# Kernel optimization log

Hardware: AMD Instinct MI355X
Metric: run time of the kernel (lower is better)

Reference implementation:

```python
import jax, jax.numpy as jnp
import numpy as np

ENC, DEC, ATT = 2048, 512, 512

def setup_inputs() -> dict:
    key = jax.random.key(0)
    ks = jax.random.split(key, 8)
    B, L = 64, 1024
    s1 = 1.0 / np.sqrt(ENC)
    s2 = 1.0 / np.sqrt(DEC)
    s3 = 1.0 / np.sqrt(ATT)
    return {
        "features": jax.random.normal(ks[0], (B, L, ENC), jnp.float32),
        "hidden_state": jax.random.normal(ks[1], (B, DEC), jnp.float32),
        "W1": jax.random.uniform(ks[2], (ENC, ATT), jnp.float32, -s1, s1),
        "b1": jax.random.uniform(ks[3], (ATT,), jnp.float32, -s1, s1),
        "W2": jax.random.uniform(ks[4], (DEC, ATT), jnp.float32, -s2, s2),
        "b2": jax.random.uniform(ks[5], (ATT,), jnp.float32, -s2, s2),
        "V": jax.random.uniform(ks[6], (ATT, 1), jnp.float32, -s3, s3),
        "bv": jax.random.uniform(ks[7], (1,), jnp.float32, -s3, s3),
    }

def reference(features, hidden_state, W1, b1, W2, b2, V, bv):
    # features: [B, L, ENC], hidden_state: [B, DEC]
    proj_f = jnp.einsum('ble,ea->bla', features, W1) + b1          # [B, L, A]
    proj_h = (hidden_state @ W2 + b2)[:, None, :]                  # [B, 1, A]
    attention_hidden = jnp.tanh(proj_f + proj_h)                   # [B, L, A]
    score = jnp.einsum('bla,ao->blo', attention_hidden, V) + bv    # [B, L, 1]
    attention_weights = jax.nn.softmax(score, axis=1)              # [B, L, 1]
    context_vector = jnp.sum(attention_weights * features, axis=1) # [B, ENC]
    return (context_vector, attention_weights)
```

## Files before the change

kernel.cpp:

```cpp
#include <hip/hip_runtime.h>
#include <stdint.h>


typedef float  f32x4 __attribute__((ext_vector_type(4)));
typedef short  s16x8 __attribute__((ext_vector_type(8)));
typedef unsigned short u16x8 __attribute__((ext_vector_type(8)));

#define AS_GLB __attribute__((address_space(1)))
#define AS_LDS __attribute__((address_space(3)))

__device__ __forceinline__ unsigned short f2bf(float f) {
    unsigned int u = __float_as_uint(f);
    u += 0x7fffu + ((u >> 16) & 1u);
    return (unsigned short)(u >> 16);
}

__device__ __forceinline__ float fast_tanh(float x) {
    return 1.0f - 2.0f / (__expf(2.0f * x) + 1.0f);
}

__global__ __launch_bounds__(256) void k_w1t(const float* __restrict__ W1,
                                             unsigned short* __restrict__ w1t) {
    __shared__ float tile[64][65];
    const int k0 = blockIdx.x * 64;
    const int n0 = blockIdx.y * 64;
    const int t = threadIdx.x, ty = t >> 6, tx = t & 63;
    #pragma unroll
    for (int i = ty; i < 64; i += 4)
        tile[i][tx] = W1[(size_t)(k0 + i) * 512 + n0 + tx];
    __syncthreads();
    #pragma unroll
    for (int i = ty; i < 64; i += 4)
        w1t[(size_t)(n0 + i) * 2048 + k0 + tx] = f2bf(tile[tx][i]);
}

__global__ __launch_bounds__(256) void k_projh(const float* __restrict__ hs,
                                               const float* __restrict__ W2,
                                               const float* __restrict__ b2,
                                               float* __restrict__ ph) {
    __shared__ float hsm[512];
    __shared__ float part[256];
    const int b = blockIdx.x, c0 = blockIdx.y * 128, t = threadIdx.x;
    hsm[t]       = hs[b * 512 + t];
    hsm[t + 256] = hs[b * 512 + t + 256];
    __syncthreads();
    const int j = c0 + (t & 127), half = t >> 7;
    float s = 0.f;
    const float* wp = W2 + (size_t)(half * 256) * 512 + j;
    const float* hp = hsm + half * 256;
    #pragma unroll 8
    for (int i = 0; i < 256; ++i) s += hp[i] * wp[(size_t)i * 512];
    part[t] = s;
    __syncthreads();
    if (t < 128) ph[b * 512 + j] = part[t] + part[t + 128] + b2[j];
}

__global__ __launch_bounds__(256, 2) void k_score(const float* __restrict__ feat,
                                                  const unsigned short* __restrict__ w1t,
                                                  const float* __restrict__ b1,
                                                  const float* __restrict__ ph,
                                                  const float* __restrict__ V,
                                                  float* __restrict__ score) {
    __shared__ __align__(16) unsigned short As[64 * 32];
    __shared__ __align__(16) unsigned short Bs[512 * 32];
    __shared__ float red[4][64];

    const int tid  = threadIdx.x;
    const int wave = tid >> 6, lane = tid & 63;
    const int quad = lane >> 4, l15 = lane & 15;
    const int m0 = blockIdx.x * 64;
    const int bb = m0 >> 10;

    const int am = tid >> 2, ac = tid & 3;
    const float* aptr = feat + (size_t)(m0 + am) * 2048 + ac * 8;
    const int asl = (am * 4 + (ac ^ ((am >> 1) & 3))) * 8;

    const int bn0 = wave * 128 + (lane >> 2);
    const int bc  = (lane & 3) ^ ((lane >> 3) & 3);
    const unsigned short* bptr = w1t + (size_t)bn0 * 2048 + bc * 8;

    f32x4 acc[4][8];
    const f32x4 zero = {0.f, 0.f, 0.f, 0.f};
    #pragma unroll
    for (int i = 0; i < 4; ++i)
        #pragma unroll
        for (int j = 0; j < 8; ++j) acc[i][j] = zero;

    f32x4 a0 = *(const f32x4*)aptr;
    f32x4 a1 = *(const f32x4*)(aptr + 4);

    for (int ks = 0; ks < 64; ++ks) {
        __syncthreads();
        u16x8 aw;
        aw[0] = f2bf(a0.x); aw[1] = f2bf(a0.y); aw[2] = f2bf(a0.z); aw[3] = f2bf(a0.w);
        aw[4] = f2bf(a1.x); aw[5] = f2bf(a1.y); aw[6] = f2bf(a1.z); aw[7] = f2bf(a1.w);
        *(u16x8*)(&As[asl]) = aw;
        const unsigned short* g = bptr + ks * 32;
        #pragma unroll
        for (int r = 0; r < 8; ++r) {
            __builtin_amdgcn_global_load_lds((const AS_GLB uint32_t*)(g + (size_t)r * 32768),
                                             (AS_LDS uint32_t*)(&Bs[(wave * 512 + r * 64) * 8]),
                                             16, 0, 0);
        }
        __syncthreads();

        if (ks < 63) {
            const float* ap = aptr + (ks + 1) * 32;
            a0 = *(const f32x4*)ap;
            a1 = *(const f32x4*)(ap + 4);
        }

        s16x8 af[4], bf[8];
        #pragma unroll
        for (int i = 0; i < 4; ++i) {
            const int m = i * 16 + l15;
            af[i] = *(const s16x8*)(&As[(m * 4 + (quad ^ ((m >> 1) & 3))) * 8]);
        }
        #pragma unroll
        for (int j = 0; j < 8; ++j) {
            const int n = wave * 128 + j * 16 + l15;
            bf[j] = *(const s16x8*)(&Bs[(n * 4 + (quad ^ ((n >> 1) & 3))) * 8]);
        }
        #pragma unroll
        for (int i = 0; i < 4; ++i)
            #pragma unroll
            for (int j = 0; j < 8; ++j)
                acc[i][j] = __builtin_amdgcn_mfma_f32_16x16x32_bf16(af[i], bf[j], acc[i][j], 0, 0, 0);
    }

    float ls[4][4];
    #pragma unroll
    for (int i = 0; i < 4; ++i)
        #pragma unroll
        for (int r = 0; r < 4; ++r) ls[i][r] = 0.f;
    #pragma unroll
    for (int j = 0; j < 8; ++j) {
        const int n = wave * 128 + j * 16 + l15;
        const float bias = b1[n] + ph[bb * 512 + n];
        const float vj = V[n];
        #pragma unroll
        for (int i = 0; i < 4; ++i)
            #pragma unroll
            for (int r = 0; r < 4; ++r)
                ls[i][r] += vj * fast_tanh(acc[i][j][r] + bias);
    }
    #pragma unroll
    for (int m = 1; m < 16; m <<= 1)
        #pragma unroll
        for (int i = 0; i < 4; ++i)
            #pragma unroll
            for (int r = 0; r < 4; ++r)
                ls[i][r] += __shfl_xor(ls[i][r], m, 64);
    if (l15 == 0) {
        #pragma unroll
        for (int i = 0; i < 4; ++i)
            #pragma unroll
            for (int r = 0; r < 4; ++r)
                red[wave][i * 16 + quad * 4 + r] = ls[i][r];
    }
    __syncthreads();
    if (tid < 64)
        score[m0 + tid] = red[0][tid] + red[1][tid] + red[2][tid] + red[3][tid];
}

__global__ __launch_bounds__(256) void k_softmax(const float* __restrict__ score,
                                                 float* __restrict__ wout,
                                                 float* __restrict__ ctx,
                                                 int zero_ctx) {
    __shared__ float sred[4];
    const int b = blockIdx.x, t = threadIdx.x;
    const int wave = t >> 6, lane = t & 63;
    float s[4];
    #pragma unroll
    for (int i = 0; i < 4; ++i) s[i] = score[b * 1024 + t + i * 256];
    float mx = fmaxf(fmaxf(s[0], s[1]), fmaxf(s[2], s[3]));
    #pragma unroll
    for (int m = 1; m < 64; m <<= 1) mx = fmaxf(mx, __shfl_xor(mx, m, 64));
    if (lane == 0) sred[wave] = mx;
    __syncthreads();
    mx = fmaxf(fmaxf(sred[0], sred[1]), fmaxf(sred[2], sred[3]));
    float e[4], sum = 0.f;
    #pragma unroll
    for (int i = 0; i < 4; ++i) { e[i] = __expf(s[i] - mx); sum += e[i]; }
    #pragma unroll
    for (int m = 1; m < 64; m <<= 1) sum += __shfl_xor(sum, m, 64);
    __syncthreads();
    if (lane == 0) sred[wave] = sum;
    __syncthreads();
    const float inv = 1.0f / (sred[0] + sred[1] + sred[2] + sred[3]);
    #pragma unroll
    for (int i = 0; i < 4; ++i) wout[b * 1024 + t + i * 256] = e[i] * inv;
    if (zero_ctx) {
        #pragma unroll
        for (int i = 0; i < 8; ++i) ctx[b * 2048 + t + i * 256] = 0.f;
    }
}

__global__ __launch_bounds__(256) void k_ctx_part(const float* __restrict__ feat,
                                                  const float* __restrict__ wgt,
                                                  float* __restrict__ part) {
    __shared__ float wl[128];
    const int b = blockIdx.x, lc = blockIdx.y, t = threadIdx.x;
    if (t < 128) wl[t] = wgt[b * 1024 + lc * 128 + t];
    __syncthreads();
    const float* fp = feat + ((size_t)b * 1024 + (size_t)lc * 128) * 2048 + t * 8;
    f32x4 a0 = {0.f, 0.f, 0.f, 0.f}, a1 = {0.f, 0.f, 0.f, 0.f};
    #pragma unroll 4
    for (int l = 0; l < 128; ++l) {
        const f32x4 f0 = *(const f32x4*)(fp + (size_t)l * 2048);
        const f32x4 f1 = *(const f32x4*)(fp + (size_t)l * 2048 + 4);
        const float w = wl[l];
        a0 += w * f0;
        a1 += w * f1;
    }
    float* pp = part + ((size_t)(b * 8 + lc)) * 2048 + t * 8;
    *(f32x4*)pp = a0;
    *(f32x4*)(pp + 4) = a1;
}

__global__ __launch_bounds__(256) void k_ctx_red(const float* __restrict__ part,
                                                 float* __restrict__ ctx) {
    const int b = blockIdx.x, t = threadIdx.x;
    const float* pp = part + (size_t)b * 8 * 2048 + t * 8;
    f32x4 s0 = {0.f, 0.f, 0.f, 0.f}, s1 = {0.f, 0.f, 0.f, 0.f};
    #pragma unroll
    for (int r = 0; r < 8; ++r) {
        s0 += *(const f32x4*)(pp + (size_t)r * 2048);
        s1 += *(const f32x4*)(pp + (size_t)r * 2048 + 4);
    }
    float* cp = ctx + b * 2048 + t * 8;
    *(f32x4*)cp = s0;
    *(f32x4*)(cp + 4) = s1;
}

__global__ __launch_bounds__(256) void k_ctx_atomic(const float* __restrict__ feat,
                                                    const float* __restrict__ wgt,
                                                    float* __restrict__ ctx) {
    __shared__ float wl[128];
    const int b = blockIdx.x, lc = blockIdx.y, t = threadIdx.x;
    if (t < 128) wl[t] = wgt[b * 1024 + lc * 128 + t];
    __syncthreads();
    const float* fp = feat + ((size_t)b * 1024 + (size_t)lc * 128) * 2048 + t * 8;
    f32x4 a0 = {0.f, 0.f, 0.f, 0.f}, a1 = {0.f, 0.f, 0.f, 0.f};
    #pragma unroll 4
    for (int l = 0; l < 128; ++l) {
        const f32x4 f0 = *(const f32x4*)(fp + (size_t)l * 2048);
        const f32x4 f1 = *(const f32x4*)(fp + (size_t)l * 2048 + 4);
        const float w = wl[l];
        a0 += w * f0;
        a1 += w * f1;
    }
    float* cp = ctx + b * 2048 + t * 8;
    atomicAdd(cp + 0, a0.x); atomicAdd(cp + 1, a0.y);
    atomicAdd(cp + 2, a0.z); atomicAdd(cp + 3, a0.w);
    atomicAdd(cp + 4, a1.x); atomicAdd(cp + 5, a1.y);
    atomicAdd(cp + 6, a1.z); atomicAdd(cp + 7, a1.w);
}

extern "C" void kernel_launch(void* const* d_in, const int* in_sizes, int n_in,
                              void* d_out, int out_size, void* d_ws, size_t ws_size,
                              hipStream_t stream) {
    const float* feat = (const float*)d_in[0];
    const float* hs   = (const float*)d_in[1];
    const float* W1   = (const float*)d_in[2];
    const float* b1   = (const float*)d_in[3];
    const float* W2   = (const float*)d_in[4];
    const float* b2   = (const float*)d_in[5];
    const float* V    = (const float*)d_in[6];

    const size_t OFF_PH    = 2u * 1024 * 1024;
    const size_t OFF_SCORE = OFF_PH + 128u * 1024;
    const size_t OFF_PART  = OFF_SCORE + 256u * 1024;
    const size_t NEED_PART = OFF_PART + (size_t)64 * 8 * 2048 * 4;

    unsigned short* w1t = (unsigned short*)d_ws;
    float* ph    = (float*)((char*)d_ws + OFF_PH);
    float* score = (float*)((char*)d_ws + OFF_SCORE);
    float* part  = (float*)((char*)d_ws + OFF_PART);

    float* ctx  = (float*)d_out;
    float* wout = ctx + 64 * 2048;

    const int use_part = (ws_size >= NEED_PART) ? 1 : 0;

    k_w1t    <<<dim3(32, 8), 256, 0, stream>>>(W1, w1t);
    k_projh  <<<dim3(64, 4), 256, 0, stream>>>(hs, W2, b2, ph);
    k_score  <<<1024,        256, 0, stream>>>(feat, w1t, b1, ph, V, score);
    k_softmax<<<64,          256, 0, stream>>>(score, wout, ctx, use_part ? 0 : 1);
    if (use_part) {
        k_ctx_part<<<dim3(64, 8), 256, 0, stream>>>(feat, wout, part);
        k_ctx_red <<<64,          256, 0, stream>>>(part, ctx);
    } else {
        k_ctx_atomic<<<dim3(64, 8), 256, 0, stream>>>(feat, wout, ctx);
    }
}
```

Measured before the change: 923.1 us.

## Double-buffer LDS in score GEMM and widen block to 128 rows with 8 waves

The score GEMM kernel now uses 512 threads arranged as 2x4 waves over a 128-row by 512-column tile. This halves how often each W1 column tile is fetched per row, and the global-to-LDS traffic per block is amortised over twice as many rows. LDS buffers for A and B are double-buffered so the next k-slice is loaded while MFMAs run on the current one, leaving one barrier per iteration instead of two. LDS use rises to roughly 82 KB per block, which may limit occupancy to one block per CU, and the 2-block launch bound at 512 threads adds register pressure with 32 accumulators per thread.

```diff
diff --git a/kernel.cpp b/kernel.cpp
--- a/kernel.cpp
+++ b/kernel.cpp
@@ -55,27 +55,28 @@
     if (t < 128) ph[b * 512 + j] = part[t] + part[t + 128] + b2[j];
 }
 
-__global__ __launch_bounds__(256, 2) void k_score(const float* __restrict__ feat,
+__global__ __launch_bounds__(512, 2) void k_score(const float* __restrict__ feat,
                                                   const unsigned short* __restrict__ w1t,
                                                   const float* __restrict__ b1,
                                                   const float* __restrict__ ph,
                                                   const float* __restrict__ V,
                                                   float* __restrict__ score) {
-    __shared__ __align__(16) unsigned short As[64 * 32];
-    __shared__ __align__(16) unsigned short Bs[512 * 32];
-    __shared__ float red[4][64];
+    __shared__ __align__(16) unsigned short As[2][128 * 32];
+    __shared__ __align__(16) unsigned short Bs[2][512 * 32];
+    __shared__ float red[8][64];
 
     const int tid  = threadIdx.x;
     const int wave = tid >> 6, lane = tid & 63;
     const int quad = lane >> 4, l15 = lane & 15;
-    const int m0 = blockIdx.x * 64;
+    const int wrow = wave >> 2, wcol = wave & 3;
+    const int m0 = blockIdx.x * 128;
     const int bb = m0 >> 10;
 
     const int am = tid >> 2, ac = tid & 3;
     const float* aptr = feat + (size_t)(m0 + am) * 2048 + ac * 8;
     const int asl = (am * 4 + (ac ^ ((am >> 1) & 3))) * 8;
 
-    const int bn0 = wave * 128 + (lane >> 2);
+    const int bn0 = wave * 64 + (lane >> 2);
     const int bc  = (lane & 3) ^ ((lane >> 3) & 3);
     const unsigned short* bptr = w1t + (size_t)bn0 * 2048 + bc * 8;
 
@@ -88,44 +89,62 @@
 
     f32x4 a0 = *(const f32x4*)aptr;
     f32x4 a1 = *(const f32x4*)(aptr + 4);
-
-    for (int ks = 0; ks < 64; ++ks) {
-        __syncthreads();
+    {
         u16x8 aw;
         aw[0] = f2bf(a0.x); aw[1] = f2bf(a0.y); aw[2] = f2bf(a0.z); aw[3] = f2bf(a0.w);
         aw[4] = f2bf(a1.x); aw[5] = f2bf(a1.y); aw[6] = f2bf(a1.z); aw[7] = f2bf(a1.w);
-        *(u16x8*)(&As[asl]) = aw;
-        const unsigned short* g = bptr + ks * 32;
-        #pragma unroll
-        for (int r = 0; r < 8; ++r) {
-            __builtin_amdgcn_global_load_lds((const AS_GLB uint32_t*)(g + (size_t)r * 32768),
-                                             (AS_LDS uint32_t*)(&Bs[(wave * 512 + r * 64) * 8]),
+        *(u16x8*)(&As[0][asl]) = aw;
+        #pragma unroll
+        for (int r = 0; r < 4; ++r) {
+            __builtin_amdgcn_global_load_lds((const AS_GLB uint32_t*)(bptr + (size_t)r * 16 * 2048),
+                                             (AS_LDS uint32_t*)(&Bs[0][(wave * 256 + r * 64) * 8]),
                                              16, 0, 0);
         }
+        a0 = *(const f32x4*)(aptr + 32);
+        a1 = *(const f32x4*)(aptr + 36);
+    }
+    __syncthreads();
+
+    for (int ks = 0; ks < 64; ++ks) {
+        const int cur = ks & 1, nxt = cur ^ 1;
+
+        if (ks < 63) {
+            u16x8 aw;
+            aw[0] = f2bf(a0.x); aw[1] = f2bf(a0.y); aw[2] = f2bf(a0.z); aw[3] = f2bf(a0.w);
+            aw[4] = f2bf(a1.x); aw[5] = f2bf(a1.y); aw[6] = f2bf(a1.z); aw[7] = f2bf(a1.w);
+            *(u16x8*)(&As[nxt][asl]) = aw;
+            const unsigned short* g = bptr + (ks + 1) * 32;
+            #pragma unroll
+            for (int r = 0; r < 4; ++r) {
+                __builtin_amdgcn_global_load_lds((const AS_GLB uint32_t*)(g + (size_t)r * 16 * 2048),
+                                                 (AS_LDS uint32_t*)(&Bs[nxt][(wave * 256 + r * 64) * 8]),
+                                                 16, 0, 0);
+            }
+            if (ks < 62) {
+                const float* ap = aptr + (ks + 2) * 32;
+                a0 = *(const f32x4*)ap;
+                a1 = *(const f32x4*)(ap + 4);
+            }
+        }
+
+        s16x8 af[4], bfr[8];
+        #pragma unroll
+        for (int i = 0; i < 4; ++i) {
+            const int m = wrow * 64 + i * 16 + l15;
+            af[i] = *(const s16x8*)(&As[cur][(m * 4 + (quad ^ ((m >> 1) & 3))) * 8]);
+        }
+        #pragma unroll
+        for (int j = 0; j < 8; ++j) {
+            const int n = wcol * 128 + j * 16 + l15;
+            bfr[j] = *(const s16x8*)(&Bs[cur][(n * 4 + (quad ^ ((n >> 1) & 3))) * 8]);
+        }
+        #pragma unroll
+        for (int i = 0; i < 4; ++i)
+            #pragma unroll
+            for (int j = 0; j < 8; ++j)
+                acc[i][j] = __builtin_amdgcn_mfma_f32_16x16x32_bf16(af[i], bfr[j], acc[i][j], 0, 0, 0);
+
         __syncthreads();
-
-        if (ks < 63) {
-            const float* ap = aptr + (ks + 1) * 32;
-            a0 = *(const f32x4*)ap;
-            a1 = *(const f32x4*)(ap + 4);
-        }
-
-        s16x8 af[4], bf[8];
-        #pragma unroll
-        for (int i = 0; i < 4; ++i) {
-            const int m = i * 16 + l15;
-            af[i] = *(const s16x8*)(&As[(m * 4 + (quad ^ ((m >> 1) & 3))) * 8]);
-        }
-        #pragma unroll
-        for (int j = 0; j < 8; ++j) {
-            const int n = wave * 128 + j * 16 + l15;
-            bf[j] = *(const s16x8*)(&Bs[(n * 4 + (quad ^ ((n >> 1) & 3))) * 8]);
-        }
-        #pragma unroll
-        for (int i = 0; i < 4; ++i)
-            #pragma unroll
-            for (int j = 0; j < 8; ++j)
-                acc[i][j] = __builtin_amdgcn_mfma_f32_16x16x32_bf16(af[i], bf[j], acc[i][j], 0, 0, 0);
     }
 
     float ls[4][4];
@@ -135,7 +154,7 @@
         for (int r = 0; r < 4; ++r) ls[i][r] = 0.f;
     #pragma unroll
     for (int j = 0; j < 8; ++j) {
-        const int n = wave * 128 + j * 16 + l15;
+        const int n = wcol * 128 + j * 16 + l15;
         const float bias = b1[n] + ph[bb * 512 + n];
         const float vj = V[n];
         #pragma unroll
@@ -159,8 +178,11 @@
                 red[wave][i * 16 + quad * 4 + r] = ls[i][r];
     }
     __syncthreads();
-    if (tid < 64)
-        score[m0 + tid] = red[0][tid] + red[1][tid] + red[2][tid] + red[3][tid];
+    if (tid < 128) {
+        const int wr = tid >> 6, x = tid & 63;
+        score[m0 + wr * 64 + x] = red[wr * 4 + 0][x] + red[wr * 4 + 1][x]
+                                + red[wr * 4 + 2][x] + red[wr * 4 + 3][x];
+    }
 }
 
 __global__ __launch_bounds__(256) void k_softmax(const float* __restrict__ score,
@@ -285,7 +307,7 @@
 
     k_w1t    <<<dim3(32, 8), 256, 0, stream>>>(W1, w1t);
     k_projh  <<<dim3(64, 4), 256, 0, stream>>>(hs, W2, b2, ph);
-    k_score  <<<1024,        256, 0, stream>>>(feat, w1t, b1, ph, V, score);
+    k_score  <<<512,         512, 0, stream>>>(feat, w1t, b1, ph, V, score);
     k_softmax<<<64,          256, 0, stream>>>(score, wout, ctx, use_part ? 0 : 1);
     if (use_part) {
         k_ctx_part<<<dim3(64, 8), 256, 0, stream>>>(feat, wout, part);
```

Result: faster. 888.7 us (-3.7%).
